# Performance work log

Hardware: AMD Instinct MI355X
Metric: run time of the kernel (lower is better)

## Reference

```python
import jax, jax.numpy as jnp
import numpy as np

S, B, V, E, H = 512, 16, 32003, 512, 512
HH = H // 2  # per-direction encoder hidden (bidirectional LSTM)


def _lstm(x, Wih, Whh, b, hsz):
    # x: (T, B, in); Wih: (4h, in); Whh: (4h, h); b: (4h,)  (PyTorch i,f,g,o gate order)
    xW = jnp.einsum('tbi,gi->tbg', x, Wih) + b  # precompute input projections
    h0 = jnp.zeros((x.shape[1], hsz), x.dtype)

    def step(carry, xt):
        h, c = carry
        g = xt + h @ Whh.T
        i, f, gg, o = jnp.split(g, 4, axis=-1)
        c = jax.nn.sigmoid(f) * c + jax.nn.sigmoid(i) * jnp.tanh(gg)
        h = jax.nn.sigmoid(o) * jnp.tanh(c)
        return (h, c), h

    _, hs = jax.lax.scan(step, (h0, h0), xW)
    return hs  # (T, B, hsz)


def setup_inputs() -> dict:
    key = jax.random.key(0)
    k = jax.random.split(key, 16)
    sc = 0.08
    return {
        'numeric': jax.random.randint(k[0], (S, B), 0, V, dtype=jnp.int32),
        'numeric_noised': jax.random.randint(k[1], (S, B), 0, V, dtype=jnp.int32),
        'emb': jax.random.normal(k[2], (V, E), jnp.float32) * sc,
        'enc_Wih_f': jax.random.normal(k[3], (4 * HH, E), jnp.float32) * sc,
        'enc_Whh_f': jax.random.normal(k[4], (4 * HH, HH), jnp.float32) * sc,
        'enc_b_f': jnp.zeros((4 * HH,), jnp.float32),
        'enc_Wih_b': jax.random.normal(k[5], (4 * HH, E), jnp.float32) * sc,
        'enc_Whh_b': jax.random.normal(k[6], (4 * HH, HH), jnp.float32) * sc,
        'enc_b_b': jnp.zeros((4 * HH,), jnp.float32),
        'dec_Wih': jax.random.normal(k[7], (4 * H, E), jnp.float32) * sc,
        'dec_Whh': jax.random.normal(k[8], (4 * H, H), jnp.float32) * sc,
        'dec_b': jnp.zeros((4 * H,), jnp.float32),
        'attn_W': jax.random.normal(k[9], (H, H), jnp.float32) * sc,
        'mlp_W': jax.random.normal(k[10], (H, 2 * H), jnp.float32) * sc,
        'mlp_b': jnp.zeros((H,), jnp.float32),
        'out_W': jax.random.normal(k[11], (V, H), jnp.float32) * sc,
        'out_b': jnp.zeros((V,), jnp.float32),
    }


def reference(numeric, numeric_noised, emb, enc_Wih_f, enc_Whh_f, enc_b_f,
              enc_Wih_b, enc_Whh_b, enc_b_b, dec_Wih, dec_Whh, dec_b,
              attn_W, mlp_W, mlp_b, out_W, out_b):
    zero = jnp.zeros((1, B), numeric.dtype)  # zeroBeginning (<SOS>=0)
    num = jnp.concatenate([zero, numeric], 0)            # (S+1, B)
    noised = jnp.concatenate([zero, numeric_noised], 0)  # (S+1, B)
    inp_t, tgt = num[:-1], num[1:]
    embedded = emb[inp_t]        # (S, B, E)
    emb_noised = emb[noised]     # (S+1, B, E)

    # BiLSTM encoder (hidden H/2 per direction)
    ef = _lstm(emb_noised, enc_Wih_f, enc_Whh_f, enc_b_f, HH)
    eb = _lstm(emb_noised[::-1], enc_Wih_b, enc_Whh_b, enc_b_b, HH)[::-1]
    enc = jnp.concatenate([ef, eb], -1)                  # (S+1, B, H)

    # LSTM decoder (teacher forced)
    dec = _lstm(embedded, dec_Wih, dec_Whh, dec_b, H)    # (S, B, H)

    # attention: scores over encoder positions s, softmax on dim s
    proj = jnp.einsum('sbh,kh->sbk', enc, attn_W)        # attention_proj (no bias)
    scores = jnp.einsum('sbh,tbh->bst', proj, dec)       # (B, S+1, S)
    attn = jax.nn.softmax(scores, axis=1)
    # context: equivalent of (enc.unsqueeze(2)*attn.unsqueeze(3)).sum(0).transpose(0,1)
    ctx = jnp.einsum('sbh,bst->tbh', enc, attn)          # (S, B, H)

    full = jnp.concatenate([dec, ctx], -1)               # (S, B, 2H)
    hid = jax.nn.relu(jnp.einsum('tbf,hf->tbh', full, mlp_W) + mlp_b)
    logits = jnp.einsum('tbh,vh->tbv', hid, out_W) + out_b
    logp = jax.nn.log_softmax(logits, -1)

    # NLLLoss with ignore_index=0, mean over non-ignored tokens
    nll = -jnp.take_along_axis(logp, tgt[..., None].astype(jnp.int32), axis=-1)[..., 0]
    mask = (tgt != 0).astype(logp.dtype)
    return (nll * mask).sum() / mask.sum()
```

## Files before the change

kernel.cpp:

```cpp
#include <hip/hip_runtime.h>
#include <stdint.h>
#include <stddef.h>


typedef __attribute__((ext_vector_type(8))) short  sx8;
typedef __attribute__((ext_vector_type(8))) __bf16 bfx8;
typedef __attribute__((ext_vector_type(4))) float  fx4;

#define NCHUNK 251

__device__ __forceinline__ float bf2f(short h) {
  unsigned u = ((unsigned)(unsigned short)h) << 16;
  return __builtin_bit_cast(float, u);
}
__device__ __forceinline__ short f2bf(float f) {
  unsigned u = __builtin_bit_cast(unsigned, f);
  u = (u + 0x7fffu + ((u >> 16) & 1u)) >> 16;
  return (short)u;
}
__device__ __forceinline__ fx4 mfma_bf16(sx8 a, sx8 b, fx4 c) {
  return __builtin_amdgcn_mfma_f32_16x16x32_bf16(
      __builtin_bit_cast(bfx8, a), __builtin_bit_cast(bfx8, b), c, 0, 0, 0);
}
__device__ __forceinline__ float sigm(float x) { return 1.f / (1.f + __expf(-x)); }
__device__ __forceinline__ float tanh_f(float x) { return 2.f / (1.f + __expf(-2.f * x)) - 1.f; }

__device__ __forceinline__ unsigned long long cp_load_u64(const void* p) {
  return __hip_atomic_load((const unsigned long long*)p,
                           __ATOMIC_RELAXED, __HIP_MEMORY_SCOPE_AGENT);
}
__device__ __forceinline__ sx8 cp_load_sx8(const void* p) {
  union { unsigned long long u[2]; sx8 v; } cvt;
  cvt.u[0] = cp_load_u64(p);
  cvt.u[1] = cp_load_u64((const char*)p + 8);
  return cvt.v;
}

__global__ void k_f32_to_bf16(const float* __restrict__ src, short* __restrict__ dst, long n) {
  long i = (long)blockIdx.x * 256 + threadIdx.x;
  long stride = (long)gridDim.x * 256;
  for (; i < n; i += stride) dst[i] = f2bf(src[i]);
}

__global__ void k_embed(const float* __restrict__ emb, const int* __restrict__ idx,
                        short* __restrict__ dst, int rows) {
  long i = (long)blockIdx.x * 256 + threadIdx.x;
  if (i >= (long)rows * 512) return;
  int r = (int)(i >> 9), c = (int)(i & 511);
  int tok = (r < 16) ? 0 : idx[r - 16];
  dst[i] = f2bf(emb[(size_t)tok * 512 + c]);
}

#define BM 128
#define BN 128
#define BK 32
__global__ __launch_bounds__(256) void k_gemm_bt(
    const short* __restrict__ A, long lda, long sA,
    const short* __restrict__ B, long ldb, long sB,
    short* __restrict__ Cb, float* __restrict__ Cf, long ldc, long sC,
    const float* __restrict__ bias, int relu,
    int M, int N, int K) {
  __shared__ short As[BM * BK];
  __shared__ short Bs[BN * BK];
  const int bz = blockIdx.z;
  const short* Ab = A + (size_t)bz * sA;
  const short* Bb = B + (size_t)bz * sB;
  const int m0 = blockIdx.x * BM, n0 = blockIdx.y * BN;
  const int tid = threadIdx.x;
  const int lane = tid & 63, wave = tid >> 6;
  const int wr = wave >> 1, wc = wave & 1;
  const int q = lane >> 4, l15 = lane & 15;
  const int sr = tid >> 2;
  const int sc = (tid & 3) * 8;

  fx4 acc[4][4] = {};

  for (int k0 = 0; k0 < K; k0 += BK) {
    __syncthreads();
    *(sx8*)&As[ sr       * BK + sc] = *(const sx8*)(Ab + (size_t)(m0 + sr)      * lda + k0 + sc);
    *(sx8*)&As[(sr + 64) * BK + sc] = *(const sx8*)(Ab + (size_t)(m0 + sr + 64) * lda + k0 + sc);
    *(sx8*)&Bs[ sr       * BK + sc] = *(const sx8*)(Bb + (size_t)(n0 + sr)      * ldb + k0 + sc);
    *(sx8*)&Bs[(sr + 64) * BK + sc] = *(const sx8*)(Bb + (size_t)(n0 + sr + 64) * ldb + k0 + sc);
    __syncthreads();
    sx8 af[4], bf[4];
#pragma unroll
    for (int i = 0; i < 4; i++) af[i] = *(const sx8*)&As[(wr * 64 + i * 16 + l15) * BK + q * 8];
#pragma unroll
    for (int j = 0; j < 4; j++) bf[j] = *(const sx8*)&Bs[(wc * 64 + j * 16 + l15) * BK + q * 8];
#pragma unroll
    for (int i = 0; i < 4; i++)
#pragma unroll
      for (int j = 0; j < 4; j++) acc[i][j] = mfma_bf16(af[i], bf[j], acc[i][j]);
  }

#pragma unroll
  for (int i = 0; i < 4; i++) {
    int row0 = m0 + wr * 64 + i * 16 + q * 4;
#pragma unroll
    for (int j = 0; j < 4; j++) {
      int col = n0 + wc * 64 + j * 16 + l15;
      if (col >= N) continue;
      float bv = bias ? bias[col] : 0.f;
#pragma unroll
      for (int r = 0; r < 4; r++) {
        int row = row0 + r;
        if (row >= M) continue;
        float v = acc[i][j][r] + bv;
        if (relu) v = fmaxf(v, 0.f);
        size_t o = (size_t)bz * sC + (size_t)row * ldc + col;
        if (Cb) Cb[o] = f2bf(v);
        else    Cf[o] = v;
      }
    }
  }
}

__global__ __launch_bounds__(256) void k_gemm_lse(
    const short* __restrict__ A, const short* __restrict__ B,
    const float* __restrict__ bias,
    float* __restrict__ mp, float* __restrict__ sp,
    int N, int K) {
  __shared__ short As[BM * BK];
  __shared__ short Bs[BN * BK];
  __shared__ float redm[2][2][64];
  __shared__ float reds[2][2][64];
  const int m0 = blockIdx.x * BM, n0 = blockIdx.y * BN;
  const int tid = threadIdx.x;
  const int lane = tid & 63, wave = tid >> 6;
  const int wr = wave >> 1, wc = wave & 1;
  const int q = lane >> 4, l15 = lane & 15;
  const int sr = tid >> 2, sc = (tid & 3) * 8;

  fx4 acc[4][4] = {};
  for (int k0 = 0; k0 < K; k0 += BK) {
    __syncthreads();
    *(sx8*)&As[ sr       * BK + sc] = *(const sx8*)(A + (size_t)(m0 + sr)      * K + k0 + sc);
    *(sx8*)&As[(sr + 64) * BK + sc] = *(const sx8*)(A + (size_t)(m0 + sr + 64) * K + k0 + sc);
    *(sx8*)&Bs[ sr       * BK + sc] = *(const sx8*)(B + (size_t)(n0 + sr)      * K + k0 + sc);
    *(sx8*)&Bs[(sr + 64) * BK + sc] = *(const sx8*)(B + (size_t)(n0 + sr + 64) * K + k0 + sc);
    __syncthreads();
    sx8 af[4], bf[4];
#pragma unroll
    for (int i = 0; i < 4; i++) af[i] = *(const sx8*)&As[(wr * 64 + i * 16 + l15) * BK + q * 8];
#pragma unroll
    for (int j = 0; j < 4; j++) bf[j] = *(const sx8*)&Bs[(wc * 64 + j * 16 + l15) * BK + q * 8];
#pragma unroll
    for (int i = 0; i < 4; i++)
#pragma unroll
      for (int j = 0; j < 4; j++) acc[i][j] = mfma_bf16(af[i], bf[j], acc[i][j]);
  }

#pragma unroll
  for (int i = 0; i < 4; i++) {
#pragma unroll
    for (int r = 0; r < 4; r++) {
      float vj[4], mx = -1e30f;
#pragma unroll
      for (int j = 0; j < 4; j++) {
        int col = n0 + wc * 64 + j * 16 + l15;
        float v = (col < N) ? (acc[i][j][r] + bias[col]) : -1e30f;
        vj[j] = v;
        mx = fmaxf(mx, v);
      }
#pragma unroll
      for (int off = 1; off < 16; off <<= 1) mx = fmaxf(mx, __shfl_xor(mx, off, 64));
      float s = 0.f;
#pragma unroll
      for (int j = 0; j < 4; j++) s += __expf(vj[j] - mx);
#pragma unroll
      for (int off = 1; off < 16; off <<= 1) s += __shfl_xor(s, off, 64);
      if (l15 == 0) {
        int rl = i * 16 + q * 4 + r;
        redm[wr][wc][rl] = mx;
        reds[wr][wc][rl] = s;
      }
    }
  }
  __syncthreads();
  if (tid < 128) {
    int wrr = tid >> 6, rl = tid & 63;
    float ma = redm[wrr][0][rl], mb = redm[wrr][1][rl];
    float M2 = fmaxf(ma, mb);
    float S2 = reds[wrr][0][rl] * __expf(ma - M2) + reds[wrr][1][rl] * __expf(mb - M2);
    int grow = m0 + wrr * 64 + rl;
    mp[(size_t)blockIdx.y * 8192 + grow] = M2;
    sp[(size_t)blockIdx.y * 8192 + grow] = S2;
  }
}

template<int NU, int NK, int HD, int T, int GRP>
__device__ __forceinline__ void lstm_body(
    const short* __restrict__ xW, const short* __restrict__ Whh,
    short* __restrict__ outb, const int ostride, const int ocol0,
    const short* __restrict__ zbuf,
    unsigned* __restrict__ flags, const int fbase, const int nb, const int gb) {
  constexpr int NT = 4 * NU;
  constexpr int N4 = 4 * HD;
  const int lane = threadIdx.x & 63, wv = threadIdx.x >> 6;
  const int q = lane >> 4, l15 = lane & 15;
  const int j0 = gb * (NU * 64) + wv * (NU * 16);

  sx8 bfr[NT][NK];
#pragma unroll
  for (int tt = 0; tt < NT; tt++) {
    const int g = tt / NU, u = tt % NU;
    const size_t wrow = (size_t)(g * HD + j0 + u * 16 + l15);
#pragma unroll
    for (int kk = 0; kk < NK; kk++)
      bfr[tt][kk] = *(const sx8*)(Whh + wrow * HD + kk * 32 + q * 8);
  }

  float cst[NU][4] = {};
  float xg[NT][4];
  {
    const int tr0 = (GRP == 2) ? (T - 1) : 0;
#pragma unroll
    for (int tt = 0; tt < NT; tt++) {
      const int g = tt / NU, u = tt % NU;
      const int cx = g * HD + j0 + u * 16 + l15;
#pragma unroll
      for (int r = 0; r < 4; r++)
        xg[tt][r] = bf2f(xW[(size_t)(tr0 * 16 + q * 4 + r) * N4 + cx]);
    }
  }

  for (int t = 0; t < T; t++) {
    const int trow = (GRP == 2) ? (T - 1 - t) : t;

    if (t > 0) {
      const unsigned tgt = (unsigned)t;
      while (true) {
        unsigned v = tgt;
        if (lane < nb)
          v = __hip_atomic_load(&flags[fbase + lane],
                                __ATOMIC_RELAXED, __HIP_MEMORY_SCOPE_AGENT);
        if (__all((int)(v >= tgt))) break;
      }
    }

    const short* hp;
    if (t == 0) hp = zbuf;
    else {
      const int prow = (GRP == 2) ? (trow + 1) : (trow - 1);
      hp = outb + (size_t)(prow * 16) * ostride + ocol0;
    }
    sx8 afr[NK];
#pragma unroll
    for (int kk = 0; kk < NK; kk++)
      afr[kk] = cp_load_sx8(hp + (size_t)l15 * ostride + kk * 32 + q * 8);

    fx4 acc[NT] = {};
#pragma unroll
    for (int kk = 0; kk < NK; kk++)
#pragma unroll
      for (int tt = 0; tt < NT; tt++)
        acc[tt] = mfma_bf16(afr[kk], bfr[tt][kk], acc[tt]);

#pragma unroll
    for (int u = 0; u < NU; u++) {
      const int colb = ocol0 + j0 + u * 16 + (l15 & ~1);
#pragma unroll
      for (int r = 0; r < 4; r++) {
        float gi = acc[0 * NU + u][r] + xg[0 * NU + u][r];
        float gf = acc[1 * NU + u][r] + xg[1 * NU + u][r];
        float gc = acc[2 * NU + u][r] + xg[2 * NU + u][r];
        float go = acc[3 * NU + u][r] + xg[3 * NU + u][r];
        float cn = sigm(gf) * cst[u][r] + sigm(gi) * tanh_f(gc);
        cst[u][r] = cn;
        unsigned mine = (unsigned)(unsigned short)f2bf(sigm(go) * tanh_f(cn));
        unsigned other = (unsigned)__shfl_xor((int)mine, 1, 64);
        if (!(l15 & 1)) {
          unsigned dw = mine | (other << 16);
          unsigned* dst = (unsigned*)(outb + (size_t)(trow * 16 + q * 4 + r) * ostride + colb);
          __hip_atomic_store(dst, dw, __ATOMIC_RELAXED, __HIP_MEMORY_SCOPE_AGENT);
        }
      }
    }

    __syncthreads();
    if (threadIdx.x == 0)
      __hip_atomic_store(&flags[fbase + gb], (unsigned)(t + 1),
                         __ATOMIC_RELAXED, __HIP_MEMORY_SCOPE_AGENT);

    if (t + 1 < T) {
      const int ntr = (GRP == 2) ? (T - 2 - t) : (t + 1);
#pragma unroll
      for (int tt = 0; tt < NT; tt++) {
        const int g = tt / NU, u = tt % NU;
        const int cx = g * HD + j0 + u * 16 + l15;
#pragma unroll
        for (int r = 0; r < 4; r++)
          xg[tt][r] = bf2f(xW[(size_t)(ntr * 16 + q * 4 + r) * N4 + cx]);
      }
    }
  }
}

__global__ __launch_bounds__(256, 1) void k_lstm(
    const short* __restrict__ xW_d, const short* __restrict__ Wh_d,
    const short* __restrict__ xW_f, const short* __restrict__ Wh_f,
    const short* __restrict__ xW_b, const short* __restrict__ Wh_b,
    short* __restrict__ full, short* __restrict__ enc,
    const short* __restrict__ zbuf, unsigned* __restrict__ flags) {
  const int blk = blockIdx.x;
  if (blk < 8)
    lstm_body<1, 16, 512, 512, 0>(xW_d, Wh_d, full, 1024, 0,   zbuf, flags, 0, 8, blk);
  else if (blk < 10)
    lstm_body<2, 8, 256, 513, 1>(xW_f, Wh_f, enc, 512, 0,   zbuf, flags, 32, 2, blk - 8);
  else
    lstm_body<2, 8, 256, 513, 2>(xW_b, Wh_b, enc, 512, 256, zbuf, flags, 64, 2, blk - 10);
}

__global__ void k_softmax(short* __restrict__ scores) {
  const int b = blockIdx.y;
  const int t = blockIdx.x * 256 + threadIdx.x;
  short* base = scores + (size_t)b * 513 * 512 + t;
  float mx = -1e30f;
  for (int s = 0; s < 513; s++) mx = fmaxf(mx, bf2f(base[s * 512]));
  float sum = 0.f;
  for (int s = 0; s < 513; s++) sum += __expf(bf2f(base[s * 512]) - mx);
  float inv = 1.f / sum;
  for (int s = 0; s < 513; s++) base[s * 512] = f2bf(__expf(bf2f(base[s * 512]) - mx) * inv);
}

__global__ void k_transpose(const short* __restrict__ in, long ldi, long sbi,
                            short* __restrict__ out, long ldo, long sbo,
                            int rows, int cols) {
  __shared__ short tile[32][33];
  const int bz = blockIdx.z;
  const int r0 = blockIdx.x * 32, c0 = blockIdx.y * 32;
  const int tx = threadIdx.x & 31, ty = threadIdx.x >> 5;
#pragma unroll
  for (int i = 0; i < 4; i++) {
    int r = r0 + ty + i * 8, c = c0 + tx;
    short v = 0;
    if (r < rows) v = in[(size_t)bz * sbi + (size_t)r * ldi + c];
    tile[ty + i * 8][tx] = v;
  }
  __syncthreads();
#pragma unroll
  for (int i = 0; i < 4; i++) {
    int oc = c0 + ty + i * 8, orr = r0 + tx;
    if (orr < rows) out[(size_t)bz * sbo + (size_t)oc * ldo + orr] = tile[tx][ty + i * 8];
  }
}

__global__ __launch_bounds__(256) void k_tl(const short* __restrict__ hid,
                                            const short* __restrict__ W,
                                            const float* __restrict__ ob,
                                            const int* __restrict__ tgt,
                                            float* __restrict__ tl) {
  const int row = blockIdx.x * 4 + (threadIdx.x >> 6);
  const int lane = threadIdx.x & 63;
  const int tv = tgt[row];
  sx8 hv = *(const sx8*)(hid + (size_t)row * 512 + lane * 8);
  sx8 wv = *(const sx8*)(W + (size_t)tv * 512 + lane * 8);
  float s = 0.f;
#pragma unroll
  for (int e = 0; e < 8; e++) s += bf2f(hv[e]) * bf2f(wv[e]);
#pragma unroll
  for (int off = 32; off >= 1; off >>= 1) s += __shfl_down(s, off, 64);
  if (lane == 0) tl[row] = s + ob[tv];
}

__global__ __launch_bounds__(256) void k_nll(const float* __restrict__ mp,
                                             const float* __restrict__ sp,
                                             const float* __restrict__ tl,
                                             const int* __restrict__ tgt,
                                             float* __restrict__ accum) {
  const int r = blockIdx.x * 256 + threadIdx.x;
  float M = -1e30f, Ssum = 0.f;
  for (int c = 0; c < NCHUNK; c++) {
    float m = mp[(size_t)c * 8192 + r];
    float s = sp[(size_t)c * 8192 + r];
    float nM = fmaxf(M, m);
    Ssum = Ssum * __expf(M - nM) + s * __expf(m - nM);
    M = nM;
  }
  float msk = (tgt[r] != 0) ? 1.f : 0.f;
  float nll = (M + logf(Ssum) - tl[r]) * msk;
#pragma unroll
  for (int off = 32; off >= 1; off >>= 1) {
    nll += __shfl_down(nll, off, 64);
    msk += __shfl_down(msk, off, 64);
  }
  if ((threadIdx.x & 63) == 0) {
    atomicAdd(&accum[0], nll);
    atomicAdd(&accum[1], msk);
  }
}

__global__ void k_final(const float* __restrict__ accum, float* __restrict__ out) {
  out[0] = accum[0] / accum[1];
}

extern "C" void kernel_launch(void* const* d_in, const int* in_sizes, int n_in,
                              void* d_out, int out_size, void* d_ws, size_t ws_size,
                              hipStream_t stream) {
  (void)in_sizes; (void)n_in; (void)out_size;
  const int*   numeric = (const int*)  d_in[0];
  const int*   noised  = (const int*)  d_in[1];
  const float* emb     = (const float*)d_in[2];
  const float* Wih_f   = (const float*)d_in[3];
  const float* Whh_f   = (const float*)d_in[4];
  const float* b_f     = (const float*)d_in[5];
  const float* Wih_b   = (const float*)d_in[6];
  const float* Whh_b   = (const float*)d_in[7];
  const float* b_b     = (const float*)d_in[8];
  const float* dWih    = (const float*)d_in[9];
  const float* dWhh    = (const float*)d_in[10];
  const float* d_bv    = (const float*)d_in[11];
  const float* attnW   = (const float*)d_in[12];
  const float* mlpW    = (const float*)d_in[13];
  const float* mlp_b   = (const float*)d_in[14];
  const float* outW    = (const float*)d_in[15];
  const float* out_b   = (const float*)d_in[16];
  float* out = (float*)d_out;

  char* w = (char*)d_ws;
  size_t off = 0;
  auto alloc = [&](size_t bytes) -> void* {
    void* p = w + off;
    off = (off + bytes + 255) & ~(size_t)255;
    return p;
  };
  short* bWih_f = (short*)alloc((size_t)1024 * 512 * 2);
  short* bWih_b = (short*)alloc((size_t)1024 * 512 * 2);
  short* bWhh_f = (short*)alloc((size_t)1024 * 256 * 2);
  short* bWhh_b = (short*)alloc((size_t)1024 * 256 * 2);
  short* bWdec  = (short*)alloc((size_t)2048 * 512 * 2);
  short* bWhhd  = (short*)alloc((size_t)2048 * 512 * 2);
  short* battnW = (short*)alloc((size_t)512 * 512 * 2);
  short* bmlpW  = (short*)alloc((size_t)512 * 1024 * 2);
  short* boutW  = (short*)alloc((size_t)32768 * 512 * 2);
  short* embedded  = (short*)alloc((size_t)8192 * 512 * 2);
  short* embnoised = (short*)alloc((size_t)8208 * 512 * 2);
  short* g_xwf     = (short*)alloc((size_t)8208 * 1024 * 2);
  short* g_xwb     = (short*)alloc((size_t)8208 * 1024 * 2);
  short* g_xwd     = (short*)alloc((size_t)8192 * 2048 * 2);
  short* enc       = (short*)alloc((size_t)8208 * 512 * 2);
  short* proj      = (short*)alloc((size_t)8208 * 512 * 2);
  short* scores    = (short*)alloc((size_t)16 * 513 * 512 * 2);
  short* attnT     = (short*)alloc((size_t)16 * 512 * 544 * 2);
  short* encT      = (short*)alloc((size_t)16 * 512 * 544 * 2);
  short* full      = (short*)alloc((size_t)8192 * 1024 * 2);
  short* hid       = (short*)alloc((size_t)8192 * 512 * 2);
  float* mpart     = (float*)alloc((size_t)NCHUNK * 8192 * 4);
  float* spart     = (float*)alloc((size_t)NCHUNK * 8192 * 4);
  float* tlv       = (float*)alloc((size_t)8192 * 4);
  size_t small_off = off;
  short*    zbuf  = (short*)alloc((size_t)16384 * 2);
  unsigned* flags = (unsigned*)alloc(4096);
  float*    accum = (float*)alloc(256);
  size_t total = off;
  if (ws_size < total) return;

  dim3 b256(256);

  hipMemsetAsync(boutW, 0, (size_t)32768 * 512 * 2, stream);
  hipMemsetAsync(attnT, 0, (size_t)16 * 512 * 544 * 2, stream);
  hipMemsetAsync(encT, 0, (size_t)16 * 512 * 544 * 2, stream);
  hipMemsetAsync(w + small_off, 0, total - small_off, stream);

  k_f32_to_bf16<<<2048, b256, 0, stream>>>(Wih_f, bWih_f, 1024L * 512);
  k_f32_to_bf16<<<2048, b256, 0, stream>>>(Wih_b, bWih_b, 1024L * 512);
  k_f32_to_bf16<<<2048, b256, 0, stream>>>(Whh_f, bWhh_f, 1024L * 256);
  k_f32_to_bf16<<<2048, b256, 0, stream>>>(Whh_b, bWhh_b, 1024L * 256);
  k_f32_to_bf16<<<2048, b256, 0, stream>>>(dWih,  bWdec,  2048L * 512);
  k_f32_to_bf16<<<2048, b256, 0, stream>>>(dWhh,  bWhhd,  2048L * 512);
  k_f32_to_bf16<<<2048, b256, 0, stream>>>(attnW, battnW, 512L * 512);
  k_f32_to_bf16<<<2048, b256, 0, stream>>>(mlpW,  bmlpW,  512L * 1024);
  k_f32_to_bf16<<<8192, b256, 0, stream>>>(outW,  boutW,  32003L * 512);

  k_embed<<<(8192 * 512 + 255) / 256, b256, 0, stream>>>(emb, numeric, embedded, 8192);
  k_embed<<<(8208 * 512 + 255) / 256, b256, 0, stream>>>(emb, noised, embnoised, 8208);

  k_gemm_bt<<<dim3(65, 8, 1), b256, 0, stream>>>(embnoised, 512, 0, bWih_f, 512, 0,
      g_xwf, nullptr, 1024, 0, b_f, 0, 8208, 1024, 512);
  k_gemm_bt<<<dim3(65, 8, 1), b256, 0, stream>>>(embnoised, 512, 0, bWih_b, 512, 0,
      g_xwb, nullptr, 1024, 0, b_b, 0, 8208, 1024, 512);
  k_gemm_bt<<<dim3(64, 16, 1), b256, 0, stream>>>(embedded, 512, 0, bWdec, 512, 0,
      g_xwd, nullptr, 2048, 0, d_bv, 0, 8192, 2048, 512);

  k_lstm<<<12, b256, 0, stream>>>(g_xwd, bWhhd, g_xwf, bWhh_f, g_xwb, bWhh_b,
                                  full, enc, zbuf, flags);

  k_gemm_bt<<<dim3(65, 4, 1), b256, 0, stream>>>(enc, 512, 0, battnW, 512, 0,
      proj, nullptr, 512, 0, nullptr, 0, 8208, 512, 512);

  k_gemm_bt<<<dim3(5, 4, 16), b256, 0, stream>>>(proj, 8192, 512, full, 16384, 1024,
      scores, nullptr, 512, (long)513 * 512, nullptr, 0, 513, 512, 512);

  k_softmax<<<dim3(2, 16), b256, 0, stream>>>(scores);

  k_transpose<<<dim3(17, 16, 16), b256, 0, stream>>>(scores, 512, (long)513 * 512,
      attnT, 544, (long)512 * 544, 513, 512);
  k_transpose<<<dim3(17, 16, 16), b256, 0, stream>>>(enc, 8192, 512,
      encT, 544, (long)512 * 544, 513, 512);

  k_gemm_bt<<<dim3(4, 4, 16), b256, 0, stream>>>(attnT, 544, (long)512 * 544,
      encT, 544, (long)512 * 544,
      full + 512, nullptr, 16384, 1024, nullptr, 0, 512, 512, 544);

  k_gemm_bt<<<dim3(64, 4, 1), b256, 0, stream>>>(full, 1024, 0, bmlpW, 1024, 0,
      hid, nullptr, 512, 0, mlp_b, 1, 8192, 512, 1024);

  k_gemm_lse<<<dim3(64, NCHUNK), b256, 0, stream>>>(hid, boutW, out_b, mpart, spart,
                                                    32003, 512);
  k_tl<<<2048, b256, 0, stream>>>(hid, boutW, out_b, numeric, tlv);
  k_nll<<<32, b256, 0, stream>>>(mpart, spart, tlv, numeric, accum);
  k_final<<<1, 1, 0, stream>>>(accum, out);
}
```

Measured before the change: 4.428 ms.

## Pin LSTM blocks to one XCC and use plain cached loads for hidden state

Launches 512 blocks and lets only the first 12 that land on XCC 0 claim LSTM roles through an atomic counter. Because every LSTM block then shares one L2, the agent-scope atomic loads and stores of the hidden state become ordinary vector loads and stores, which cuts latency on the serial recurrence. This relies on all 12 claimed blocks being resident on XCC 0 at once and on cache coherence within one XCC. A spin budget now bounds the flag wait, so a stall ends the wait instead of hanging, and the compute may then read stale data. The role counter in flags[96] also has to be reset before each launch.

```diff
diff --git a/kernel.cpp b/kernel.cpp
--- a/kernel.cpp
+++ b/kernel.cpp
@@ -25,15 +25,10 @@
 __device__ __forceinline__ float sigm(float x) { return 1.f / (1.f + __expf(-x)); }
 __device__ __forceinline__ float tanh_f(float x) { return 2.f / (1.f + __expf(-2.f * x)) - 1.f; }
 
-__device__ __forceinline__ unsigned long long cp_load_u64(const void* p) {
-  return __hip_atomic_load((const unsigned long long*)p,
-                           __ATOMIC_RELAXED, __HIP_MEMORY_SCOPE_AGENT);
-}
-__device__ __forceinline__ sx8 cp_load_sx8(const void* p) {
-  union { unsigned long long u[2]; sx8 v; } cvt;
-  cvt.u[0] = cp_load_u64(p);
-  cvt.u[1] = cp_load_u64((const char*)p + 8);
-  return cvt.v;
+__device__ __forceinline__ int xcc_id() {
+  unsigned x;
+  asm("s_getreg_b32 %0, hwreg(HW_REG_XCC_ID)" : "=s"(x));
+  return (int)(x & 0xf);
 }
 
 __global__ void k_f32_to_bf16(const float* __restrict__ src, short* __restrict__ dst, long n) {
@@ -199,6 +194,7 @@
   const int lane = threadIdx.x & 63, wv = threadIdx.x >> 6;
   const int q = lane >> 4, l15 = lane & 15;
   const int j0 = gb * (NU * 64) + wv * (NU * 16);
+  unsigned budget = 1u << 23;
 
   sx8 bfr[NT][NK];
 #pragma unroll
@@ -229,13 +225,15 @@
 
     if (t > 0) {
       const unsigned tgt = (unsigned)t;
-      while (true) {
+      while (budget) {
         unsigned v = tgt;
         if (lane < nb)
           v = __hip_atomic_load(&flags[fbase + lane],
                                 __ATOMIC_RELAXED, __HIP_MEMORY_SCOPE_AGENT);
         if (__all((int)(v >= tgt))) break;
+        --budget;
       }
+      asm volatile("" ::: "memory");
     }
 
     const short* hp;
@@ -247,7 +245,7 @@
     sx8 afr[NK];
 #pragma unroll
     for (int kk = 0; kk < NK; kk++)
-      afr[kk] = cp_load_sx8(hp + (size_t)l15 * ostride + kk * 32 + q * 8);
+      afr[kk] = *(const sx8*)(hp + (size_t)l15 * ostride + kk * 32 + q * 8);
 
     fx4 acc[NT] = {};
 #pragma unroll
@@ -271,8 +269,7 @@
         unsigned other = (unsigned)__shfl_xor((int)mine, 1, 64);
         if (!(l15 & 1)) {
           unsigned dw = mine | (other << 16);
-          unsigned* dst = (unsigned*)(outb + (size_t)(trow * 16 + q * 4 + r) * ostride + colb);
-          __hip_atomic_store(dst, dw, __ATOMIC_RELAXED, __HIP_MEMORY_SCOPE_AGENT);
+          *(unsigned*)(outb + (size_t)(trow * 16 + q * 4 + r) * ostride + colb) = dw;
         }
       }
     }
@@ -302,13 +299,24 @@
     const short* __restrict__ xW_b, const short* __restrict__ Wh_b,
     short* __restrict__ full, short* __restrict__ enc,
     const short* __restrict__ zbuf, unsigned* __restrict__ flags) {
-  const int blk = blockIdx.x;
-  if (blk < 8)
-    lstm_body<1, 16, 512, 512, 0>(xW_d, Wh_d, full, 1024, 0,   zbuf, flags, 0, 8, blk);
-  else if (blk < 10)
-    lstm_body<2, 8, 256, 513, 1>(xW_f, Wh_f, enc, 512, 0,   zbuf, flags, 32, 2, blk - 8);
+  __shared__ int role_s;
+  if (threadIdx.x == 0) {
+    int r = -1;
+    if (xcc_id() == 0) {
+      unsigned c = atomicAdd(&flags[96], 1u);
+      if (c < 12u) r = (int)c;
+    }
+    role_s = r;
+  }
+  __syncthreads();
+  const int role = role_s;
+  if (role < 0) return;
+  if (role < 8)
+    lstm_body<1, 16, 512, 512, 0>(xW_d, Wh_d, full, 1024, 0,   zbuf, flags, 0, 8, role);
+  else if (role < 10)
+    lstm_body<2, 8, 256, 513, 1>(xW_f, Wh_f, enc, 512, 0,   zbuf, flags, 32, 2, role - 8);
   else
-    lstm_body<2, 8, 256, 513, 2>(xW_b, Wh_b, enc, 512, 256, zbuf, flags, 64, 2, blk - 10);
+    lstm_body<2, 8, 256, 513, 2>(xW_b, Wh_b, enc, 512, 256, zbuf, flags, 64, 2, role - 10);
 }
 
 __global__ void k_softmax(short* __restrict__ scores) {
@@ -482,8 +490,8 @@
   k_gemm_bt<<<dim3(64, 16, 1), b256, 0, stream>>>(embedded, 512, 0, bWdec, 512, 0,
       g_xwd, nullptr, 2048, 0, d_bv, 0, 8192, 2048, 512);
 
-  k_lstm<<<12, b256, 0, stream>>>(g_xwd, bWhhd, g_xwf, bWhh_f, g_xwb, bWhh_b,
-                                  full, enc, zbuf, flags);
+  k_lstm<<<512, b256, 0, stream>>>(g_xwd, bWhhd, g_xwf, bWhh_f, g_xwb, bWhh_b,
+                                   full, enc, zbuf, flags);
 
   k_gemm_bt<<<dim3(65, 4, 1), b256, 0, stream>>>(enc, 512, 0, battnW, 512, 0,
       proj, nullptr, 512, 0, nullptr, 0, 8208, 512, 512);
```

After: 4.710 ms. 6.4% more time.
